# Kernel optimization log

Measured on AMD Instinct MI355X. Metric: run time of the kernel, lower is better.

The kernel has to match this reference:

```python
import jax, jax.numpy as jnp
import numpy as np

EEG_DIM, CLIP_DIM, NUM_SUBJECTS, BATCH = 256, 512, 13, 16384
EPS = 1e-12  # torch F.normalize eps


def setup_inputs() -> dict:
    key = jax.random.key(0)
    k0, k1, k2, k3, k4, k5 = jax.random.split(key, 6)
    # Kaiming-uniform-ish init for per-subject Linear layers
    lim1 = 1.0 / np.sqrt(EEG_DIM)
    lim2 = 1.0 / np.sqrt(CLIP_DIM)
    return {
        "eeg_emb": jax.random.normal(k0, (BATCH, EEG_DIM), dtype=jnp.float32),
        "subject_ids": jax.random.randint(k1, (BATCH,), 0, NUM_SUBJECTS),
        "W1": jax.random.uniform(k2, (NUM_SUBJECTS, EEG_DIM, CLIP_DIM), jnp.float32, -lim1, lim1),
        "b1": jax.random.uniform(k3, (NUM_SUBJECTS, CLIP_DIM), jnp.float32, -lim1, lim1),
        "W2": jax.random.uniform(k4, (NUM_SUBJECTS, CLIP_DIM, CLIP_DIM), jnp.float32, -lim2, lim2),
        "b2": jax.random.uniform(k5, (NUM_SUBJECTS, CLIP_DIM), jnp.float32, -lim2, lim2),
    }


def reference(eeg_emb, subject_ids, W1, b1, W2, b2):
    # Hard-routed per-subject 2-layer MLP. We compute all subject heads densely
    # (b s h) and select the row for each sample's subject id -- vectorized
    # equivalent of the original per-subject gather/scatter loop.
    h = jax.nn.relu(jnp.einsum('bd,sdh->bsh', eeg_emb, W1) + b1)  # [B,S,H]
    y = jnp.einsum('bsh,sho->bso', h, W2) + b2                     # [B,S,O]
    out = jnp.take_along_axis(y, subject_ids[:, None, None], axis=1)[:, 0, :]  # [B,O]
    # F.normalize(p=2, dim=1): x / max(||x||, eps)
    norm = jnp.linalg.norm(out, axis=1, keepdims=True)
    return out / jnp.maximum(norm, EPS)
```

## Files before the change

kernel.cpp:

```cpp
#include <hip/hip_runtime.h>
#include <hip/hip_bf16.h>


#define BATCH 16384
#define EEG 256
#define CLIP 512
#define NSUB 13

#define M_BCNT 0
#define M_SOFF 832
#define M_TOT  846
#define M_C112 859
#define M_IDX  896

typedef unsigned short u16;
typedef __attribute__((ext_vector_type(8))) short short8;
typedef __attribute__((ext_vector_type(4))) float f32x4;

__device__ __forceinline__ u16 f2bf(float f) {
    union { float f; unsigned int u; } v; v.f = f;
    unsigned int u = v.u;
    unsigned int r = (u + 0x7FFFu + ((u >> 16) & 1u)) >> 16;
    return (u16)r;
}

__global__ __launch_bounds__(256) void convert_pack(
    const float* __restrict__ W1, const float* __restrict__ W2,
    u16* __restrict__ w1p, u16* __restrict__ w2p,
    const int* __restrict__ sid, int* __restrict__ meta) {
    __shared__ u16 T[64][72];
    __shared__ int hh[NSUB];
    int b = blockIdx.x;
    const float* src; u16* dstbase; int ksteps;
    int s, kt, g;
    if (b < 416) {
        s = b >> 5; int t = b & 31;
        kt = t >> 3; g = t & 7;
        ksteps = 8;
        src = W1 + (size_t)s * EEG * CLIP;
        dstbase = w1p + (size_t)s * CLIP * EEG;
    } else {
        b -= 416; s = b >> 6; int t = b & 63;
        kt = t >> 3; g = t & 7;
        ksteps = 16;
        src = W2 + (size_t)s * CLIP * CLIP;
        dstbase = w2p + (size_t)s * CLIP * CLIP;
    }
    int k0 = kt << 6, n0 = g << 6;
    int tid = threadIdx.x;
    int rk = tid >> 2;
    int cg = (tid & 3) << 4;
    const float4* p4 = reinterpret_cast<const float4*>(src + (size_t)(k0 + rk) * CLIP + n0 + cg);
    #pragma unroll
    for (int jj = 0; jj < 4; ++jj) {
        float4 v = p4[jj];
        T[cg + jj * 4 + 0][rk] = f2bf(v.x);
        T[cg + jj * 4 + 1][rk] = f2bf(v.y);
        T[cg + jj * 4 + 2][rk] = f2bf(v.z);
        T[cg + jj * 4 + 3][rk] = f2bf(v.w);
    }
    __syncthreads();
    int colin = tid & 63, sl = (tid >> 6) & 3;
    #pragma unroll
    for (int half = 0; half < 2; ++half) {
        int t = kt * 2 + half;
        u16* dst = dstbase + ((size_t)(g * ksteps + t)) * 2048 + sl * 512 + colin * 8;
        *reinterpret_cast<short8*>(dst) =
            *reinterpret_cast<const short8*>(&T[colin][half * 32 + sl * 8]);
    }
    if (blockIdx.x < 64) {
        if (tid < NSUB) hh[tid] = 0;
        __syncthreads();
        atomicAdd(&hh[sid[blockIdx.x * 256 + tid]], 1);
        __syncthreads();
        if (tid < NSUB) meta[M_BCNT + blockIdx.x * NSUB + tid] = hh[tid];
    }
}

__global__ __launch_bounds__(256) void scanscatter_k(
    const int* __restrict__ sid, int* __restrict__ meta) {
    __shared__ int cnt[64][NSUB];
    __shared__ int so[NSUB + 1], myoff[NSUB], tot[NSUB];
    __shared__ int h[NSUB];
    int tid = threadIdx.x;
    for (int i = tid; i < 64 * NSUB; i += 256)
        cnt[i / NSUB][i % NSUB] = meta[M_BCNT + i];
    if (tid < NSUB) h[tid] = 0;
    __syncthreads();
    if (tid < NSUB) {
        int run = 0, mine = 0;
        for (int b = 0; b < 64; ++b) {
            if (b == (int)blockIdx.x) mine = run;
            run += cnt[b][tid];
        }
        tot[tid] = run; myoff[tid] = mine;
    }
    __syncthreads();
    if (tid == 0) {
        int off = 0;
        for (int s = 0; s < NSUB; ++s) { so[s] = off; off += tot[s]; }
        so[NSUB] = off;
    }
    __syncthreads();
    if (blockIdx.x == 0) {
        if (tid < NSUB + 1) meta[M_SOFF + tid] = so[tid];
        if (tid < NSUB) meta[M_TOT + tid] = tot[tid];
        if (tid == 0) {
            int c112 = 0;
            for (int s = 0; s < NSUB; ++s) {
                meta[M_C112 + s] = c112;
                c112 += (tot[s] + 111) / 112;
            }
            meta[M_C112 + NSUB] = c112;
        }
    }
    int i = blockIdx.x * 256 + tid;
    int s = sid[i];
    int r = atomicAdd(&h[s], 1);
    meta[M_IDX + so[s] + myoff[s] + r] = i;
}

__global__ __launch_bounds__(512) void mlp_k(
    const float* __restrict__ X, const float* __restrict__ b1,
    const float* __restrict__ b2, const u16* __restrict__ w1p,
    const u16* __restrict__ w2p, const int* __restrict__ meta,
    float* __restrict__ out) {

    __shared__ u16 Hs[112 * 520];
    __shared__ u16 Wl[8 * 2048];
    __shared__ float partial[112 * 8];
    __shared__ float scalev[112];
    __shared__ int info[4];
    __shared__ int rowidx[112];
    __shared__ int cobuf[14], sobuf[14], totbuf[NSUB];

    int tid = threadIdx.x;

    int nwg = gridDim.x;
    int q = nwg >> 3, r = nwg & 7;
    int xcd = blockIdx.x & 7, idx = blockIdx.x >> 3;
    int bid = (xcd < r) ? xcd * (q + 1) + idx : r * (q + 1) + (xcd - r) * q + idx;

    if (tid < 14) { cobuf[tid] = meta[M_C112 + tid]; sobuf[tid] = meta[M_SOFF + tid]; }
    if (tid < NSUB) totbuf[tid] = meta[M_TOT + tid];
    __syncthreads();
    if (tid == 0) {
        int total = cobuf[NSUB];
        if (bid < total) {
            int s = 0;
            while (s < NSUB && !(bid >= cobuf[s] && bid < cobuf[s + 1])) s++;
            int chunk = bid - cobuf[s];
            info[0] = s;
            info[1] = sobuf[s] + chunk * 112;
            info[2] = min(112, totbuf[s] - chunk * 112);
        } else info[0] = -1;
    }
    __syncthreads();
    if (info[0] < 0) return;
    int s = info[0], rowbase = info[1], nrows = info[2];
    if (tid < 112) rowidx[tid] = meta[M_IDX + rowbase + min(tid, nrows - 1)];

    int wave = tid >> 6, lane = tid & 63;
    int c = lane & 15, gl = lane >> 4;
    int col0 = wave * 64;
    const u16* w1c = w1p + (size_t)s * CLIP * EEG + (size_t)wave * 8 * 2048;
    const u16* w2c = w2p + (size_t)s * CLIP * CLIP + (size_t)wave * 16 * 2048;
    u16* wl = &Wl[wave * 2048];

#define STAGE_LDS(srcp) do {                                                     \
        _Pragma("unroll")                                                        \
        for (int _it = 0; _it < 4; ++_it)                                        \
            __builtin_amdgcn_global_load_lds(                                    \
                (const __attribute__((address_space(1))) unsigned int*)          \
                    ((srcp) + _it * 512 + lane * 8),                             \
                (__attribute__((address_space(3))) unsigned int*)(wl + _it * 512), \
                16, 0, 0);                                                       \
    } while (0)

    u16* Xc = Hs;

    f32x4 acc[7][4];
    #pragma unroll
    for (int mi = 0; mi < 7; ++mi)
        #pragma unroll
        for (int ni = 0; ni < 4; ++ni)
            acc[mi][ni] = (f32x4){0.f, 0.f, 0.f, 0.f};

    int srow = min(tid >> 2, 111), sq4 = tid & 3;

    for (int kc = 0; kc < 4; ++kc) {
        __syncthreads();
        {
            const float4* xp = reinterpret_cast<const float4*>(
                X + (size_t)rowidx[srow] * EEG) + kc * 16 + sq4 * 4;
            u16* xd = &Xc[srow * 72 + sq4 * 16];
            #pragma unroll
            for (int j = 0; j < 4; ++j) {
                float4 v = xp[j];
                union { u16 u[4]; uint2 qq; } pk;
                pk.u[0] = f2bf(v.x); pk.u[1] = f2bf(v.y);
                pk.u[2] = f2bf(v.z); pk.u[3] = f2bf(v.w);
                *reinterpret_cast<uint2*>(&xd[j * 4]) = pk.qq;
            }
        }
        __syncthreads();
        #pragma unroll
        for (int half = 0; half < 2; ++half) {
            int t = kc * 2 + half;
            STAGE_LDS(w1c + (size_t)t * 2048);
            asm volatile("s_waitcnt vmcnt(0)" ::: "memory");
            __builtin_amdgcn_sched_barrier(0);
            short8 bb[4], a[7];
            #pragma unroll
            for (int ni = 0; ni < 4; ++ni)
                bb[ni] = *reinterpret_cast<const short8*>(&wl[gl * 512 + (ni * 16 + c) * 8]);
            #pragma unroll
            for (int mi = 0; mi < 7; ++mi)
                a[mi] = *reinterpret_cast<const short8*>(
                    &Xc[(mi * 16 + c) * 72 + half * 32 + gl * 8]);
            #pragma unroll
            for (int mi = 0; mi < 7; ++mi)
                #pragma unroll
                for (int ni = 0; ni < 4; ++ni)
                    acc[mi][ni] = __builtin_amdgcn_mfma_f32_16x16x32_bf16(a[mi], bb[ni], acc[mi][ni], 0, 0, 0);
        }
    }
    __syncthreads();

    {
        float bias1[4];
        #pragma unroll
        for (int ni = 0; ni < 4; ++ni) bias1[ni] = b1[s * CLIP + col0 + ni * 16 + c];
        #pragma unroll
        for (int mi = 0; mi < 7; ++mi)
            #pragma unroll
            for (int ni = 0; ni < 4; ++ni)
                #pragma unroll
                for (int i = 0; i < 4; ++i) {
                    float h = fmaxf(acc[mi][ni][i] + bias1[ni], 0.f);
                    Hs[(mi * 16 + gl * 4 + i) * 520 + col0 + ni * 16 + c] = f2bf(h);
                }
    }
    __syncthreads();

    #pragma unroll
    for (int mi = 0; mi < 7; ++mi)
        #pragma unroll
        for (int ni = 0; ni < 4; ++ni)
            acc[mi][ni] = (f32x4){0.f, 0.f, 0.f, 0.f};

    STAGE_LDS(w2c);
    for (int t = 0; t < 16; ++t) {
        asm volatile("s_waitcnt vmcnt(0)" ::: "memory");
        __builtin_amdgcn_sched_barrier(0);
        short8 bb[4];
        #pragma unroll
        for (int ni = 0; ni < 4; ++ni)
            bb[ni] = *reinterpret_cast<const short8*>(&wl[gl * 512 + (ni * 16 + c) * 8]);
        asm volatile("s_waitcnt lgkmcnt(0)" ::: "memory");
        __builtin_amdgcn_sched_barrier(0);
        if (t < 15) STAGE_LDS(w2c + (size_t)(t + 1) * 2048);
        short8 a[7];
        #pragma unroll
        for (int mi = 0; mi < 7; ++mi)
            a[mi] = *reinterpret_cast<const short8*>(
                &Hs[(mi * 16 + c) * 520 + t * 32 + gl * 8]);
        #pragma unroll
        for (int mi = 0; mi < 7; ++mi)
            #pragma unroll
            for (int ni = 0; ni < 4; ++ni)
                acc[mi][ni] = __builtin_amdgcn_mfma_f32_16x16x32_bf16(a[mi], bb[ni], acc[mi][ni], 0, 0, 0);
    }
#undef STAGE_LDS

    float sq[7][4];
    {
        float bias2[4];
        #pragma unroll
        for (int ni = 0; ni < 4; ++ni) bias2[ni] = b2[s * CLIP + col0 + ni * 16 + c];
        #pragma unroll
        for (int mi = 0; mi < 7; ++mi)
            #pragma unroll
            for (int i = 0; i < 4; ++i) sq[mi][i] = 0.f;
        #pragma unroll
        for (int mi = 0; mi < 7; ++mi)
            #pragma unroll
            for (int ni = 0; ni < 4; ++ni)
                #pragma unroll
                for (int i = 0; i < 4; ++i) {
                    float v = acc[mi][ni][i] + bias2[ni];
                    acc[mi][ni][i] = v;
                    sq[mi][i] += v * v;
                }
    }
    #pragma unroll
    for (int m = 1; m < 16; m <<= 1)
        #pragma unroll
        for (int mi = 0; mi < 7; ++mi)
            #pragma unroll
            for (int i = 0; i < 4; ++i)
                sq[mi][i] += __shfl_xor(sq[mi][i], m);

    if (c == 0) {
        #pragma unroll
        for (int mi = 0; mi < 7; ++mi)
            #pragma unroll
            for (int i = 0; i < 4; ++i)
                partial[(mi * 16 + gl * 4 + i) * 8 + wave] = sq[mi][i];
    }
    __syncthreads();
    if (tid < 112) {
        float t = 0.f;
        #pragma unroll
        for (int w = 0; w < 8; ++w) t += partial[tid * 8 + w];
        scalev[tid] = 1.f / fmaxf(sqrtf(t), 1e-12f);
    }
    __syncthreads();

    #pragma unroll
    for (int mi = 0; mi < 7; ++mi)
        #pragma unroll
        for (int i = 0; i < 4; ++i) {
            int row = mi * 16 + gl * 4 + i;
            if (row < nrows) {
                float sc = scalev[row];
                float* op = out + (size_t)rowidx[row] * CLIP + col0 + c;
                #pragma unroll
                for (int ni = 0; ni < 4; ++ni)
                    __builtin_nontemporal_store(acc[mi][ni][i] * sc, op + ni * 16);
            }
        }
}

extern "C" void kernel_launch(void* const* d_in, const int* in_sizes, int n_in,
                              void* d_out, int out_size, void* d_ws, size_t ws_size,
                              hipStream_t stream) {
    const float* eeg = (const float*)d_in[0];
    const int* sid   = (const int*)d_in[1];
    const float* W1  = (const float*)d_in[2];
    const float* b1  = (const float*)d_in[3];
    const float* W2  = (const float*)d_in[4];
    const float* b2  = (const float*)d_in[5];
    float* out = (float*)d_out;

    u16* w1p = (u16*)d_ws;
    u16* w2p = w1p + (size_t)NSUB * CLIP * EEG;
    int* meta = (int*)(w2p + (size_t)NSUB * CLIP * CLIP);

    convert_pack<<<1248, 256, 0, stream>>>(W1, W2, w1p, w2p, sid, meta);
    scanscatter_k<<<64, 256, 0, stream>>>(sid, meta);
    mlp_k<<<BATCH / 112 + NSUB + 1, 512, 0, stream>>>(eeg, b1, b2, w1p, w2p, meta, out);
}
```

Measured before the change: 51.30 us.

## Double-buffer weight staging across both GEMMs and shrink row tile to 80

Replaces the single LDS weight buffer with a per-wave double buffer and a continuous prefetch stream that spans W1 and then W2 chunks. Each chunk's global-to-LDS load is now overlapped with MFMA on the previous chunk instead of waiting on vmcnt(0). The row tile drops from 112 to 80, which launches more workgroups and cuts accumulator registers and LDS use. Full __syncthreads are replaced by raw s_barrier with only lgkmcnt waits so prefetches stay in flight. The trade-off is less weight reuse per workgroup, more total weight traffic, and more fragile manual wait counts.

```diff
diff --git a/kernel.cpp b/kernel.cpp
--- a/kernel.cpp
+++ b/kernel.cpp
@@ -10,7 +10,7 @@
 #define M_BCNT 0
 #define M_SOFF 832
 #define M_TOT  846
-#define M_C112 859
+#define M_C80  859
 #define M_IDX  896
 
 typedef unsigned short u16;
@@ -22,6 +22,13 @@
     unsigned int u = v.u;
     unsigned int r = (u + 0x7FFFu + ((u >> 16) & 1u)) >> 16;
     return (u16)r;
+}
+
+__device__ __forceinline__ void raw_barrier_lgkm() {
+    asm volatile("s_waitcnt lgkmcnt(0)" ::: "memory");
+    __builtin_amdgcn_sched_barrier(0);
+    __builtin_amdgcn_s_barrier();
+    __builtin_amdgcn_sched_barrier(0);
 }
 
 __global__ __launch_bounds__(256) void convert_pack(
@@ -106,12 +113,12 @@
         if (tid < NSUB + 1) meta[M_SOFF + tid] = so[tid];
         if (tid < NSUB) meta[M_TOT + tid] = tot[tid];
         if (tid == 0) {
-            int c112 = 0;
+            int c80 = 0;
             for (int s = 0; s < NSUB; ++s) {
-                meta[M_C112 + s] = c112;
-                c112 += (tot[s] + 111) / 112;
+                meta[M_C80 + s] = c80;
+                c80 += (tot[s] + 79) / 80;
             }
-            meta[M_C112 + NSUB] = c112;
+            meta[M_C80 + NSUB] = c80;
         }
     }
     int i = blockIdx.x * 256 + tid;
@@ -126,12 +133,12 @@
     const u16* __restrict__ w2p, const int* __restrict__ meta,
     float* __restrict__ out) {
 
-    __shared__ u16 Hs[112 * 520];
-    __shared__ u16 Wl[8 * 2048];
-    __shared__ float partial[112 * 8];
-    __shared__ float scalev[112];
+    __shared__ u16 Hs[80 * 520];
+    __shared__ u16 Wl[8 * 4096];
+    __shared__ float partial[80 * 8];
+    __shared__ float scalev[80];
     __shared__ int info[4];
-    __shared__ int rowidx[112];
+    __shared__ int rowidx[80];
     __shared__ int cobuf[14], sobuf[14], totbuf[NSUB];
 
     int tid = threadIdx.x;
@@ -141,7 +148,7 @@
     int xcd = blockIdx.x & 7, idx = blockIdx.x >> 3;
     int bid = (xcd < r) ? xcd * (q + 1) + idx : r * (q + 1) + (xcd - r) * q + idx;
 
-    if (tid < 14) { cobuf[tid] = meta[M_C112 + tid]; sobuf[tid] = meta[M_SOFF + tid]; }
+    if (tid < 14) { cobuf[tid] = meta[M_C80 + tid]; sobuf[tid] = meta[M_SOFF + tid]; }
     if (tid < NSUB) totbuf[tid] = meta[M_TOT + tid];
     __syncthreads();
     if (tid == 0) {
@@ -151,45 +158,51 @@
             while (s < NSUB && !(bid >= cobuf[s] && bid < cobuf[s + 1])) s++;
             int chunk = bid - cobuf[s];
             info[0] = s;
-            info[1] = sobuf[s] + chunk * 112;
-            info[2] = min(112, totbuf[s] - chunk * 112);
+            info[1] = sobuf[s] + chunk * 80;
+            info[2] = min(80, totbuf[s] - chunk * 80);
         } else info[0] = -1;
     }
     __syncthreads();
     if (info[0] < 0) return;
     int s = info[0], rowbase = info[1], nrows = info[2];
-    if (tid < 112) rowidx[tid] = meta[M_IDX + rowbase + min(tid, nrows - 1)];
+    if (tid < 80) rowidx[tid] = meta[M_IDX + rowbase + min(tid, nrows - 1)];
 
     int wave = tid >> 6, lane = tid & 63;
     int c = lane & 15, gl = lane >> 4;
     int col0 = wave * 64;
     const u16* w1c = w1p + (size_t)s * CLIP * EEG + (size_t)wave * 8 * 2048;
     const u16* w2c = w2p + (size_t)s * CLIP * CLIP + (size_t)wave * 16 * 2048;
-    u16* wl = &Wl[wave * 2048];
-
-#define STAGE_LDS(srcp) do {                                                     \
+    u16* wl = &Wl[wave * 4096];
+
+#define STAGE_G(g) do {                                                          \
+        const u16* _src = ((g) < 8) ? (w1c + (size_t)(g) * 2048)                 \
+                                    : (w2c + (size_t)((g) - 8) * 2048);          \
+        u16* _dst = wl + (((g) & 1) ? 2048 : 0);                                 \
         _Pragma("unroll")                                                        \
         for (int _it = 0; _it < 4; ++_it)                                        \
             __builtin_amdgcn_global_load_lds(                                    \
                 (const __attribute__((address_space(1))) unsigned int*)          \
-                    ((srcp) + _it * 512 + lane * 8),                             \
-                (__attribute__((address_space(3))) unsigned int*)(wl + _it * 512), \
+                    (_src + _it * 512 + lane * 8),                               \
+                (__attribute__((address_space(3))) unsigned int*)(_dst + _it * 512), \
                 16, 0, 0);                                                       \
     } while (0)
 
+    STAGE_G(0);
+    STAGE_G(1);
+
     u16* Xc = Hs;
 
-    f32x4 acc[7][4];
-    #pragma unroll
-    for (int mi = 0; mi < 7; ++mi)
+    f32x4 acc[5][4];
+    #pragma unroll
+    for (int mi = 0; mi < 5; ++mi)
         #pragma unroll
         for (int ni = 0; ni < 4; ++ni)
             acc[mi][ni] = (f32x4){0.f, 0.f, 0.f, 0.f};
 
-    int srow = min(tid >> 2, 111), sq4 = tid & 3;
+    int srow = min(tid >> 2, 79), sq4 = tid & 3;
 
     for (int kc = 0; kc < 4; ++kc) {
-        __syncthreads();
+        raw_barrier_lgkm();
         {
             const float4* xp = reinterpret_cast<const float4*>(
                 X + (size_t)rowidx[srow] * EEG) + kc * 16 + sq4 * 4;
@@ -203,36 +216,40 @@
                 *reinterpret_cast<uint2*>(&xd[j * 4]) = pk.qq;
             }
         }
-        __syncthreads();
+        raw_barrier_lgkm();
         #pragma unroll
         for (int half = 0; half < 2; ++half) {
             int t = kc * 2 + half;
-            STAGE_LDS(w1c + (size_t)t * 2048);
-            asm volatile("s_waitcnt vmcnt(0)" ::: "memory");
+            asm volatile("s_waitcnt vmcnt(4)" ::: "memory");
             __builtin_amdgcn_sched_barrier(0);
-            short8 bb[4], a[7];
+            short8 bb[4];
+            u16* wb = wl + ((t & 1) ? 2048 : 0);
             #pragma unroll
             for (int ni = 0; ni < 4; ++ni)
-                bb[ni] = *reinterpret_cast<const short8*>(&wl[gl * 512 + (ni * 16 + c) * 8]);
-            #pragma unroll
-            for (int mi = 0; mi < 7; ++mi)
+                bb[ni] = *reinterpret_cast<const short8*>(&wb[gl * 512 + (ni * 16 + c) * 8]);
+            asm volatile("s_waitcnt lgkmcnt(0)" ::: "memory");
+            __builtin_amdgcn_sched_barrier(0);
+            STAGE_G(t + 2);
+            short8 a[5];
+            #pragma unroll
+            for (int mi = 0; mi < 5; ++mi)
                 a[mi] = *reinterpret_cast<const short8*>(
                     &Xc[(mi * 16 + c) * 72 + half * 32 + gl * 8]);
             #pragma unroll
-            for (int mi = 0; mi < 7; ++mi)
+            for (int mi = 0; mi < 5; ++mi)
                 #pragma unroll
                 for (int ni = 0; ni < 4; ++ni)
                     acc[mi][ni] = __builtin_amdgcn_mfma_f32_16x16x32_bf16(a[mi], bb[ni], acc[mi][ni], 0, 0, 0);
         }
     }
-    __syncthreads();
+    raw_barrier_lgkm();
 
     {
         float bias1[4];
         #pragma unroll
         for (int ni = 0; ni < 4; ++ni) bias1[ni] = b1[s * CLIP + col0 + ni * 16 + c];
         #pragma unroll
-        for (int mi = 0; mi < 7; ++mi)
+        for (int mi = 0; mi < 5; ++mi)
             #pragma unroll
             for (int ni = 0; ni < 4; ++ni)
                 #pragma unroll
@@ -241,49 +258,50 @@
                     Hs[(mi * 16 + gl * 4 + i) * 520 + col0 + ni * 16 + c] = f2bf(h);
                 }
     }
-    __syncthreads();
-
-    #pragma unroll
-    for (int mi = 0; mi < 7; ++mi)
+    raw_barrier_lgkm();
+
+    #pragma unroll
+    for (int mi = 0; mi < 5; ++mi)
         #pragma unroll
         for (int ni = 0; ni < 4; ++ni)
             acc[mi][ni] = (f32x4){0.f, 0.f, 0.f, 0.f};
 
-    STAGE_LDS(w2c);
-    for (int t = 0; t < 16; ++t) {
-        asm volatile("s_waitcnt vmcnt(0)" ::: "memory");
+    for (int tt = 0; tt < 16; ++tt) {
+        if (tt < 15) asm volatile("s_waitcnt vmcnt(4)" ::: "memory");
+        else         asm volatile("s_waitcnt vmcnt(0)" ::: "memory");
         __builtin_amdgcn_sched_barrier(0);
         short8 bb[4];
+        u16* wb = wl + ((tt & 1) ? 2048 : 0);
         #pragma unroll
         for (int ni = 0; ni < 4; ++ni)
-            bb[ni] = *reinterpret_cast<const short8*>(&wl[gl * 512 + (ni * 16 + c) * 8]);
+            bb[ni] = *reinterpret_cast<const short8*>(&wb[gl * 512 + (ni * 16 + c) * 8]);
         asm volatile("s_waitcnt lgkmcnt(0)" ::: "memory");
         __builtin_amdgcn_sched_barrier(0);
-        if (t < 15) STAGE_LDS(w2c + (size_t)(t + 1) * 2048);
-        short8 a[7];
-        #pragma unroll
-        for (int mi = 0; mi < 7; ++mi)
+        if (tt <= 13) STAGE_G(10 + tt);
+        short8 a[5];
+        #pragma unroll
+        for (int mi = 0; mi < 5; ++mi)
             a[mi] = *reinterpret_cast<const short8*>(
-                &Hs[(mi * 16 + c) * 520 + t * 32 + gl * 8]);
-        #pragma unroll
-        for (int mi = 0; mi < 7; ++mi)
+                &Hs[(mi * 16 + c) * 520 + tt * 32 + gl * 8]);
+        #pragma unroll
+        for (int mi = 0; mi < 5; ++mi)
             #pragma unroll
             for (int ni = 0; ni < 4; ++ni)
                 acc[mi][ni] = __builtin_amdgcn_mfma_f32_16x16x32_bf16(a[mi], bb[ni], acc[mi][ni], 0, 0, 0);
     }
-#undef STAGE_LDS
-
-    float sq[7][4];
+#undef STAGE_G
+
+    float sq[5][4];
     {
         float bias2[4];
         #pragma unroll
         for (int ni = 0; ni < 4; ++ni) bias2[ni] = b2[s * CLIP + col0 + ni * 16 + c];
         #pragma unroll
-        for (int mi = 0; mi < 7; ++mi)
+        for (int mi = 0; mi < 5; ++mi)
             #pragma unroll
             for (int i = 0; i < 4; ++i) sq[mi][i] = 0.f;
         #pragma unroll
-        for (int mi = 0; mi < 7; ++mi)
+        for (int mi = 0; mi < 5; ++mi)
             #pragma unroll
             for (int ni = 0; ni < 4; ++ni)
                 #pragma unroll
@@ -296,20 +314,20 @@
     #pragma unroll
     for (int m = 1; m < 16; m <<= 1)
         #pragma unroll
-        for (int mi = 0; mi < 7; ++mi)
+        for (int mi = 0; mi < 5; ++mi)
             #pragma unroll
             for (int i = 0; i < 4; ++i)
                 sq[mi][i] += __shfl_xor(sq[mi][i], m);
 
     if (c == 0) {
         #pragma unroll
-        for (int mi = 0; mi < 7; ++mi)
+        for (int mi = 0; mi < 5; ++mi)
             #pragma unroll
             for (int i = 0; i < 4; ++i)
                 partial[(mi * 16 + gl * 4 + i) * 8 + wave] = sq[mi][i];
     }
     __syncthreads();
-    if (tid < 112) {
+    if (tid < 80) {
         float t = 0.f;
         #pragma unroll
         for (int w = 0; w < 8; ++w) t += partial[tid * 8 + w];
@@ -318,7 +336,7 @@
     __syncthreads();
 
     #pragma unroll
-    for (int mi = 0; mi < 7; ++mi)
+    for (int mi = 0; mi < 5; ++mi)
         #pragma unroll
         for (int i = 0; i < 4; ++i) {
             int row = mi * 16 + gl * 4 + i;
@@ -349,5 +367,5 @@
 
     convert_pack<<<1248, 256, 0, stream>>>(W1, W2, w1p, w2p, sid, meta);
     scanscatter_k<<<64, 256, 0, stream>>>(sid, meta);
-    mlp_k<<<BATCH / 112 + NSUB + 1, 512, 0, stream>>>(eeg, b1, b2, w1p, w2p, meta, out);
-}
+    mlp_k<<<BATCH / 80 + NSUB + 1, 512, 0, stream>>>(eeg, b1, b2, w1p, w2p, meta, out);
+}
```

Result: faster. 44.12 us (-14.0%).
